# Optimization experiments

Hardware: AMD Instinct MI355X
Metric: run time of the kernel (lower is better)

## Reference

```python
import jax, jax.numpy as jnp
import numpy as np

IN_F = 4096
OUT_F = 4096
B, S = 4, 2048
RMS_EPS = 1e-6
Q_EPS = 1e-5


def setup_inputs() -> dict:
    key = jax.random.key(0)
    kx, kw, kb, ks = jax.random.split(key, 4)
    x = jax.random.normal(kx, (B, S, IN_F), dtype=jnp.float32)
    # ternary BitNet weight in {-1, 0, +1}, stored as float32 for the reference
    W = (jax.random.randint(kw, (OUT_F, IN_F), 0, 3) - 1).astype(jnp.float32)
    rms_weight = jnp.ones((IN_F,), dtype=jnp.float32)
    bias = jax.random.normal(kb, (OUT_F,), dtype=jnp.float32)
    weight_scale = jax.random.uniform(ks, (1,), dtype=jnp.float32) + 0.5
    return {"x": x, "W": W, "rms_weight": rms_weight, "bias": bias,
            "weight_scale": weight_scale}


def reference(x, W, rms_weight, bias, weight_scale):
    # RMSNorm (self.rms_norm applied before quantized matmul)
    var = jnp.mean(x * x, axis=-1, keepdims=True)
    h = x * jax.lax.rsqrt(var + RMS_EPS) * rms_weight
    # BitNet act_quant: per-token absmax int8 quantization
    scale = 127.0 / jnp.clip(jnp.max(jnp.abs(h), axis=-1, keepdims=True), Q_EPS)  # [B,S,1]
    q = jnp.clip(jnp.round(h * scale), -128.0, 127.0)
    # ternary GEMV per token, then dequant
    y = jnp.einsum('bsk,ok->bso', q, W) / scale  # [B,S,OUT_F]
    y = y + bias
    y = y * weight_scale  # weight_scale_mode == 'multiply'
    return y
```

## Files before the change

### kernel.cpp

```cpp
#include <hip/hip_runtime.h>

#define IN_F 4096
#define OUT_F 4096
#define NTOK 8192
#define KDIM 4096

using i32x4 = __attribute__((ext_vector_type(4))) int;
using f32x4 = __attribute__((ext_vector_type(4))) float;

__device__ __forceinline__ void gload_lds16(const void* g, void* l) {
  __builtin_amdgcn_global_load_lds(
      (const __attribute__((address_space(1))) void*)g,
      (__attribute__((address_space(3))) void*)l, 16, 0, 0);
}

#define WAITV(n) asm volatile("s_waitcnt vmcnt(" #n ")" ::: "memory")
#define BAR() do { asm volatile("" ::: "memory"); __builtin_amdgcn_s_barrier(); \
                   asm volatile("" ::: "memory"); } while (0)

__global__ __launch_bounds__(256) void rmsq_kernel(
    const float* __restrict__ x, const float* __restrict__ rmsw,
    signed char* __restrict__ q, float* __restrict__ dscale) {
  const int tok = blockIdx.x;
  const int tid = threadIdx.x;
  const f32x4* xr = (const f32x4*)(x + (size_t)tok * IN_F);
  const f32x4* wr = (const f32x4*)rmsw;

  f32x4 v[4];
  float ss = 0.f;
#pragma unroll
  for (int c = 0; c < 4; ++c) {
    v[c] = xr[c * 256 + tid];
    ss += v[c].x * v[c].x + v[c].y * v[c].y + v[c].z * v[c].z + v[c].w * v[c].w;
  }

  __shared__ float red[4];
#pragma unroll
  for (int off = 32; off > 0; off >>= 1) ss += __shfl_down(ss, off, 64);
  const int wid = tid >> 6;
  if ((tid & 63) == 0) red[wid] = ss;
  __syncthreads();
  const float tot = red[0] + red[1] + red[2] + red[3];
  const float rinv = rsqrtf(tot * (1.0f / IN_F) + 1e-6f);

  f32x4 h[4];
  float amax = 0.f;
#pragma unroll
  for (int c = 0; c < 4; ++c) {
    f32x4 w = wr[c * 256 + tid];
    h[c].x = v[c].x * rinv * w.x;
    h[c].y = v[c].y * rinv * w.y;
    h[c].z = v[c].z * rinv * w.z;
    h[c].w = v[c].w * rinv * w.w;
    amax = fmaxf(amax, fabsf(h[c].x));
    amax = fmaxf(amax, fabsf(h[c].y));
    amax = fmaxf(amax, fabsf(h[c].z));
    amax = fmaxf(amax, fabsf(h[c].w));
  }

  __syncthreads();
#pragma unroll
  for (int off = 32; off > 0; off >>= 1)
    amax = fmaxf(amax, __shfl_down(amax, off, 64));
  if ((tid & 63) == 0) red[wid] = amax;
  __syncthreads();
  amax = fmaxf(fmaxf(red[0], red[1]), fmaxf(red[2], red[3]));
  amax = fmaxf(amax, 1e-5f);
  const float qs = 127.0f / amax;
  if (tid == 0) dscale[tok] = amax * (1.0f / 127.0f);

  uint* qo = (uint*)(q + (size_t)tok * IN_F);
#pragma unroll
  for (int c = 0; c < 4; ++c) {
    float r0 = fminf(fmaxf(rintf(h[c].x * qs), -128.f), 127.f);
    float r1 = fminf(fmaxf(rintf(h[c].y * qs), -128.f), 127.f);
    float r2 = fminf(fmaxf(rintf(h[c].z * qs), -128.f), 127.f);
    float r3 = fminf(fmaxf(rintf(h[c].w * qs), -128.f), 127.f);
    uint p = ((uint)((int)r0 & 255)) | ((uint)((int)r1 & 255) << 8) |
             ((uint)((int)r2 & 255) << 16) | ((uint)((int)r3 & 255) << 24);
    qo[c * 256 + tid] = p;
  }
}

__global__ __launch_bounds__(256) void wconv_kernel(
    const float* __restrict__ W, signed char* __restrict__ Wq) {
  const int idx = blockIdx.x * 256 + threadIdx.x;
  f32x4 w = ((const f32x4*)W)[idx];
  uint p = ((uint)((int)w.x & 255)) | ((uint)((int)w.y & 255) << 8) |
           ((uint)((int)w.z & 255) << 16) | ((uint)((int)w.w & 255) << 24);
  ((uint*)Wq)[idx] = p;
}

#define BM 128
#define BN 256
#define BK 64
#define NT (KDIM / BK)
#define ATILEB (BM * BK)
#define BTILEB (BN * BK)
#define BUFB (ATILEB + BTILEB)
#define NBUF 3

__global__ __launch_bounds__(256, 2) void gemm_kernel(
    const signed char* __restrict__ A, const signed char* __restrict__ Bw,
    const float* __restrict__ dscale, const float* __restrict__ bias,
    const float* __restrict__ wscale_p, float* __restrict__ out) {
  __shared__ __align__(16) signed char lds[NBUF * BUFB];

  const int tid = threadIdx.x;
  const int lane = tid & 63;
  const int wc = tid >> 6;

  const int bid = blockIdx.x;
  const int swz = (bid & 7) * 128 + (bid >> 3);
  const int m0 = (swz & 63) * BM;
  const int n0 = (swz >> 6) * BN;

  const int cA0 = tid, cA1 = tid + 256;
  const int rA0 = cA0 >> 2, rA1 = cA1 >> 2;
  const int sA0 = (cA0 & 3) ^ ((rA0 >> 1) & 3);
  const int sA1 = (cA1 & 3) ^ ((rA1 >> 1) & 3);
  const signed char* agp0 = A + (size_t)(m0 + rA0) * KDIM + sA0 * 16;
  const signed char* agp1 = A + (size_t)(m0 + rA1) * KDIM + sA1 * 16;
  const int rB = tid >> 2;
  const signed char* bgp[4];
#pragma unroll
  for (int j = 0; j < 4; ++j) {
    const int rBj = rB + j * 64;
    const int sBj = (tid & 3) ^ ((rBj >> 1) & 3);
    bgp[j] = Bw + (size_t)(n0 + rBj) * KDIM + sBj * 16;
  }

#define STAGE(kt, boff)                                                    \
  do {                                                                     \
    const int k0_ = (kt) * BK;                                             \
    signed char* lb_ = &lds[(boff)];                                       \
    gload_lds16(agp0 + k0_, lb_ + cA0 * 16);                               \
    gload_lds16(agp1 + k0_, lb_ + cA1 * 16);                               \
    gload_lds16(bgp[0] + k0_, lb_ + ATILEB + (tid + 0 * 256) * 16);        \
    gload_lds16(bgp[1] + k0_, lb_ + ATILEB + (tid + 1 * 256) * 16);        \
    gload_lds16(bgp[2] + k0_, lb_ + ATILEB + (tid + 2 * 256) * 16);        \
    gload_lds16(bgp[3] + k0_, lb_ + ATILEB + (tid + 3 * 256) * 16);        \
  } while (0)

  const int fr = lane & 15;
  const int ks = lane >> 4;
  int offA[8], offB[4];
#pragma unroll
  for (int mi = 0; mi < 8; ++mi) {
    const int row = mi * 16 + fr;
    offA[mi] = row * BK + ((ks ^ ((row >> 1) & 3)) * 16);
  }
#pragma unroll
  for (int ni = 0; ni < 4; ++ni) {
    const int row = wc * 64 + ni * 16 + fr;
    offB[ni] = ATILEB + row * BK + ((ks ^ ((row >> 1) & 3)) * 16);
  }

  i32x4 acc[8][4];
#pragma unroll
  for (int i = 0; i < 8; ++i)
#pragma unroll
    for (int j = 0; j < 4; ++j) acc[i][j] = (i32x4){0, 0, 0, 0};

  STAGE(0, 0);
  STAGE(1, BUFB);

  int br = 0;
  int bs = 2 * BUFB;
  for (int t = 0; t < NT; ++t) {
    if (t < NT - 1) WAITV(6); else WAITV(0);
    BAR();

    const signed char* bp = &lds[br];
    i32x4 af[8], bf[4];
#pragma unroll
    for (int mi = 0; mi < 8; ++mi) af[mi] = *(const i32x4*)(bp + offA[mi]);
#pragma unroll
    for (int ni = 0; ni < 4; ++ni) bf[ni] = *(const i32x4*)(bp + offB[ni]);

    if (t + 2 < NT) STAGE(t + 2, bs);

    __builtin_amdgcn_s_setprio(1);
#pragma unroll
    for (int mi = 0; mi < 8; ++mi)
#pragma unroll
      for (int ni = 0; ni < 4; ++ni)
        acc[mi][ni] = __builtin_amdgcn_mfma_i32_16x16x64_i8(af[mi], bf[ni],
                                                            acc[mi][ni], 0, 0, 0);
    __builtin_amdgcn_s_setprio(0);

    br += BUFB; if (br == NBUF * BUFB) br = 0;
    bs += BUFB; if (bs == NBUF * BUFB) bs = 0;
  }

  const float wsc = wscale_p[0];
  const int rbase = (lane >> 4) * 4;
  float bv[4];
#pragma unroll
  for (int ni = 0; ni < 4; ++ni) bv[ni] = bias[n0 + wc * 64 + ni * 16 + fr];
#pragma unroll
  for (int mi = 0; mi < 8; ++mi) {
#pragma unroll
    for (int r = 0; r < 4; ++r) {
      const int m = m0 + mi * 16 + rbase + r;
      const float ds = dscale[m];
      float* orow = out + (size_t)m * OUT_F + n0 + wc * 64;
#pragma unroll
      for (int ni = 0; ni < 4; ++ni) {
        orow[ni * 16 + fr] = ((float)acc[mi][ni][r] * ds + bv[ni]) * wsc;
      }
    }
  }
#undef STAGE
}

extern "C" void kernel_launch(void* const* d_in, const int* in_sizes, int n_in,
                              void* d_out, int out_size, void* d_ws, size_t ws_size,
                              hipStream_t stream) {
  const float* x = (const float*)d_in[0];
  const float* W = (const float*)d_in[1];
  const float* rmsw = (const float*)d_in[2];
  const float* bias = (const float*)d_in[3];
  const float* wscale = (const float*)d_in[4];
  float* out = (float*)d_out;

  signed char* q = (signed char*)d_ws;
  signed char* Wq = q + (size_t)NTOK * IN_F;
  float* dscale = (float*)(Wq + (size_t)OUT_F * IN_F);

  rmsq_kernel<<<NTOK, 256, 0, stream>>>(x, rmsw, q, dscale);
  wconv_kernel<<<(OUT_F * IN_F / 4) / 256, 256, 0, stream>>>(W, Wq);
  gemm_kernel<<<(NTOK / BM) * (OUT_F / BN), 256, 0, stream>>>(q, Wq, dscale,
                                                              bias, wscale, out);
}
```

Baseline: 192.0 us.

## Load B fragments directly from global into registers, stage only A in LDS

Each wave reads a disjoint 64-row slice of the weight tile, so staging B through shared memory gave no reuse. The change drops B from LDS and loads each wave's B fragments straight from global memory into registers, prefetched one k-step ahead. The freed LDS gives the A tile a fourth buffer and a three-stage prefetch. This removes the LDS write and read traffic for B. In exchange, global-load latency is exposed with only one iteration of lookahead, and the B loads are small, scattered 16-byte-per-lane reads that rely on cache hits.

```diff
diff --git a/kernel.cpp b/kernel.cpp
--- a/kernel.cpp
+++ b/kernel.cpp
@@ -96,15 +96,13 @@
 #define BK 64
 #define NT (KDIM / BK)
 #define ATILEB (BM * BK)
-#define BTILEB (BN * BK)
-#define BUFB (ATILEB + BTILEB)
-#define NBUF 3
+#define NBUF 4
 
 __global__ __launch_bounds__(256, 2) void gemm_kernel(
     const signed char* __restrict__ A, const signed char* __restrict__ Bw,
     const float* __restrict__ dscale, const float* __restrict__ bias,
     const float* __restrict__ wscale_p, float* __restrict__ out) {
-  __shared__ __align__(16) signed char lds[NBUF * BUFB];
+  __shared__ __align__(16) signed char lds[NBUF * ATILEB];
 
   const int tid = threadIdx.x;
   const int lane = tid & 63;
@@ -121,40 +119,28 @@
   const int sA1 = (cA1 & 3) ^ ((rA1 >> 1) & 3);
   const signed char* agp0 = A + (size_t)(m0 + rA0) * KDIM + sA0 * 16;
   const signed char* agp1 = A + (size_t)(m0 + rA1) * KDIM + sA1 * 16;
-  const int rB = tid >> 2;
-  const signed char* bgp[4];
-#pragma unroll
-  for (int j = 0; j < 4; ++j) {
-    const int rBj = rB + j * 64;
-    const int sBj = (tid & 3) ^ ((rBj >> 1) & 3);
-    bgp[j] = Bw + (size_t)(n0 + rBj) * KDIM + sBj * 16;
-  }
-
-#define STAGE(kt, boff)                                                    \
+
+#define STAGE_A(kt, boff)                                                  \
   do {                                                                     \
     const int k0_ = (kt) * BK;                                             \
     signed char* lb_ = &lds[(boff)];                                       \
     gload_lds16(agp0 + k0_, lb_ + cA0 * 16);                               \
     gload_lds16(agp1 + k0_, lb_ + cA1 * 16);                               \
-    gload_lds16(bgp[0] + k0_, lb_ + ATILEB + (tid + 0 * 256) * 16);        \
-    gload_lds16(bgp[1] + k0_, lb_ + ATILEB + (tid + 1 * 256) * 16);        \
-    gload_lds16(bgp[2] + k0_, lb_ + ATILEB + (tid + 2 * 256) * 16);        \
-    gload_lds16(bgp[3] + k0_, lb_ + ATILEB + (tid + 3 * 256) * 16);        \
   } while (0)
 
   const int fr = lane & 15;
   const int ks = lane >> 4;
-  int offA[8], offB[4];
+  int offA[8];
 #pragma unroll
   for (int mi = 0; mi < 8; ++mi) {
     const int row = mi * 16 + fr;
     offA[mi] = row * BK + ((ks ^ ((row >> 1) & 3)) * 16);
   }
-#pragma unroll
-  for (int ni = 0; ni < 4; ++ni) {
-    const int row = wc * 64 + ni * 16 + fr;
-    offB[ni] = ATILEB + row * BK + ((ks ^ ((row >> 1) & 3)) * 16);
-  }
+
+  const signed char* bgl[4];
+#pragma unroll
+  for (int ni = 0; ni < 4; ++ni)
+    bgl[ni] = Bw + (size_t)(n0 + wc * 64 + ni * 16 + fr) * KDIM + ks * 16;
 
   i32x4 acc[8][4];
 #pragma unroll
@@ -162,35 +148,49 @@
 #pragma unroll
     for (int j = 0; j < 4; ++j) acc[i][j] = (i32x4){0, 0, 0, 0};
 
-  STAGE(0, 0);
-  STAGE(1, BUFB);
+  STAGE_A(0, 0);
+  STAGE_A(1, ATILEB);
+  STAGE_A(2, 2 * ATILEB);
+  i32x4 bcur0 = *(const i32x4*)(bgl[0]);
+  i32x4 bcur1 = *(const i32x4*)(bgl[1]);
+  i32x4 bcur2 = *(const i32x4*)(bgl[2]);
+  i32x4 bcur3 = *(const i32x4*)(bgl[3]);
 
   int br = 0;
-  int bs = 2 * BUFB;
+  int bs = 3 * ATILEB;
   for (int t = 0; t < NT; ++t) {
-    if (t < NT - 1) WAITV(6); else WAITV(0);
+    WAITV(8);
     BAR();
 
     const signed char* bp = &lds[br];
-    i32x4 af[8], bf[4];
+    i32x4 af[8];
 #pragma unroll
     for (int mi = 0; mi < 8; ++mi) af[mi] = *(const i32x4*)(bp + offA[mi]);
-#pragma unroll
-    for (int ni = 0; ni < 4; ++ni) bf[ni] = *(const i32x4*)(bp + offB[ni]);
-
-    if (t + 2 < NT) STAGE(t + 2, bs);
+
+    i32x4 bn0, bn1, bn2, bn3;
+    if (t + 1 < NT) {
+      const int ko = (t + 1) * BK;
+      bn0 = *(const i32x4*)(bgl[0] + ko);
+      bn1 = *(const i32x4*)(bgl[1] + ko);
+      bn2 = *(const i32x4*)(bgl[2] + ko);
+      bn3 = *(const i32x4*)(bgl[3] + ko);
+    }
+
+    if (t + 3 < NT) STAGE_A(t + 3, bs);
 
     __builtin_amdgcn_s_setprio(1);
 #pragma unroll
-    for (int mi = 0; mi < 8; ++mi)
-#pragma unroll
-      for (int ni = 0; ni < 4; ++ni)
-        acc[mi][ni] = __builtin_amdgcn_mfma_i32_16x16x64_i8(af[mi], bf[ni],
-                                                            acc[mi][ni], 0, 0, 0);
+    for (int mi = 0; mi < 8; ++mi) {
+      acc[mi][0] = __builtin_amdgcn_mfma_i32_16x16x64_i8(af[mi], bcur0, acc[mi][0], 0, 0, 0);
+      acc[mi][1] = __builtin_amdgcn_mfma_i32_16x16x64_i8(af[mi], bcur1, acc[mi][1], 0, 0, 0);
+      acc[mi][2] = __builtin_amdgcn_mfma_i32_16x16x64_i8(af[mi], bcur2, acc[mi][2], 0, 0, 0);
+      acc[mi][3] = __builtin_amdgcn_mfma_i32_16x16x64_i8(af[mi], bcur3, acc[mi][3], 0, 0, 0);
+    }
     __builtin_amdgcn_s_setprio(0);
 
-    br += BUFB; if (br == NBUF * BUFB) br = 0;
-    bs += BUFB; if (bs == NBUF * BUFB) bs = 0;
+    bcur0 = bn0; bcur1 = bn1; bcur2 = bn2; bcur3 = bn3;
+    br += ATILEB; if (br == NBUF * ATILEB) br = 0;
+    bs += ATILEB; if (bs == NBUF * ATILEB) bs = 0;
   }
 
   const float wsc = wscale_p[0];
@@ -211,7 +211,7 @@
       }
     }
   }
-#undef STAGE
+#undef STAGE_A
 }
 
 extern "C" void kernel_launch(void* const* d_in, const int* in_sizes, int n_in,
```

New measurement: 224.5 us. 16.9% more time.

## Use two waves per GEMM block with 128x128 warp tiles

Applied to the files above, without the earlier changes.

The GEMM block drops from four waves to two, so each wave now computes a 128x128 output tile (8x8 MFMA accumulators) instead of 128x64. Each thread issues twice as many global-to-LDS loads per stage, and the vmcnt wait is adjusted to match. The aim is more MFMA work per LDS fragment read and fewer LDS reads overall. In exchange, accumulator register use doubles (256 VGPRs of accumulators alone), which may force use of AGPRs or spilling, and fewer waves are resident to hide latency.

```diff
diff --git a/kernel.cpp b/kernel.cpp
--- a/kernel.cpp
+++ b/kernel.cpp
@@ -100,7 +100,7 @@
 #define BUFB (ATILEB + BTILEB)
 #define NBUF 3
 
-__global__ __launch_bounds__(256, 2) void gemm_kernel(
+__global__ __launch_bounds__(128, 1) void gemm_kernel(
     const signed char* __restrict__ A, const signed char* __restrict__ Bw,
     const float* __restrict__ dscale, const float* __restrict__ bias,
     const float* __restrict__ wscale_p, float* __restrict__ out) {
@@ -115,52 +115,60 @@
   const int m0 = (swz & 63) * BM;
   const int n0 = (swz >> 6) * BN;
 
-  const int cA0 = tid, cA1 = tid + 256;
-  const int rA0 = cA0 >> 2, rA1 = cA1 >> 2;
-  const int sA0 = (cA0 & 3) ^ ((rA0 >> 1) & 3);
-  const int sA1 = (cA1 & 3) ^ ((rA1 >> 1) & 3);
-  const signed char* agp0 = A + (size_t)(m0 + rA0) * KDIM + sA0 * 16;
-  const signed char* agp1 = A + (size_t)(m0 + rA1) * KDIM + sA1 * 16;
-  const int rB = tid >> 2;
-  const signed char* bgp[4];
+  const signed char* agp[4];
 #pragma unroll
   for (int j = 0; j < 4; ++j) {
-    const int rBj = rB + j * 64;
-    const int sBj = (tid & 3) ^ ((rBj >> 1) & 3);
-    bgp[j] = Bw + (size_t)(n0 + rBj) * KDIM + sBj * 16;
+    const int u = tid + j * 128;
+    const int r = u >> 2;
+    const int s = (u & 3) ^ ((r >> 1) & 3);
+    agp[j] = A + (size_t)(m0 + r) * KDIM + s * 16;
+  }
+  const signed char* bgp[8];
+#pragma unroll
+  for (int j = 0; j < 8; ++j) {
+    const int u = tid + j * 128;
+    const int r = u >> 2;
+    const int s = (u & 3) ^ ((r >> 1) & 3);
+    bgp[j] = Bw + (size_t)(n0 + r) * KDIM + s * 16;
   }
 
 #define STAGE(kt, boff)                                                    \
   do {                                                                     \
     const int k0_ = (kt) * BK;                                             \
     signed char* lb_ = &lds[(boff)];                                       \
-    gload_lds16(agp0 + k0_, lb_ + cA0 * 16);                               \
-    gload_lds16(agp1 + k0_, lb_ + cA1 * 16);                               \
-    gload_lds16(bgp[0] + k0_, lb_ + ATILEB + (tid + 0 * 256) * 16);        \
-    gload_lds16(bgp[1] + k0_, lb_ + ATILEB + (tid + 1 * 256) * 16);        \
-    gload_lds16(bgp[2] + k0_, lb_ + ATILEB + (tid + 2 * 256) * 16);        \
-    gload_lds16(bgp[3] + k0_, lb_ + ATILEB + (tid + 3 * 256) * 16);        \
+    gload_lds16(agp[0] + k0_, lb_ + (tid + 0 * 128) * 16);                 \
+    gload_lds16(agp[1] + k0_, lb_ + (tid + 1 * 128) * 16);                 \
+    gload_lds16(agp[2] + k0_, lb_ + (tid + 2 * 128) * 16);                 \
+    gload_lds16(agp[3] + k0_, lb_ + (tid + 3 * 128) * 16);                 \
+    gload_lds16(bgp[0] + k0_, lb_ + ATILEB + (tid + 0 * 128) * 16);        \
+    gload_lds16(bgp[1] + k0_, lb_ + ATILEB + (tid + 1 * 128) * 16);        \
+    gload_lds16(bgp[2] + k0_, lb_ + ATILEB + (tid + 2 * 128) * 16);        \
+    gload_lds16(bgp[3] + k0_, lb_ + ATILEB + (tid + 3 * 128) * 16);        \
+    gload_lds16(bgp[4] + k0_, lb_ + ATILEB + (tid + 4 * 128) * 16);        \
+    gload_lds16(bgp[5] + k0_, lb_ + ATILEB + (tid + 5 * 128) * 16);        \
+    gload_lds16(bgp[6] + k0_, lb_ + ATILEB + (tid + 6 * 128) * 16);        \
+    gload_lds16(bgp[7] + k0_, lb_ + ATILEB + (tid + 7 * 128) * 16);        \
   } while (0)
 
   const int fr = lane & 15;
   const int ks = lane >> 4;
-  int offA[8], offB[4];
+  int offA[8], offB[8];
 #pragma unroll
   for (int mi = 0; mi < 8; ++mi) {
     const int row = mi * 16 + fr;
-    offA[mi] = row * BK + ((ks ^ ((row >> 1) & 3)) * 16);
-  }
-#pragma unroll
-  for (int ni = 0; ni < 4; ++ni) {
-    const int row = wc * 64 + ni * 16 + fr;
-    offB[ni] = ATILEB + row * BK + ((ks ^ ((row >> 1) & 3)) * 16);
-  }
-
-  i32x4 acc[8][4];
+    offA[mi] = (row * 4 + (ks ^ ((row >> 1) & 3))) * 16;
+  }
+#pragma unroll
+  for (int ni = 0; ni < 8; ++ni) {
+    const int row = wc * 128 + ni * 16 + fr;
+    offB[ni] = ATILEB + (row * 4 + (ks ^ ((row >> 1) & 3))) * 16;
+  }
+
+  i32x4 acc[8][8];
 #pragma unroll
   for (int i = 0; i < 8; ++i)
 #pragma unroll
-    for (int j = 0; j < 4; ++j) acc[i][j] = (i32x4){0, 0, 0, 0};
+    for (int j = 0; j < 8; ++j) acc[i][j] = (i32x4){0, 0, 0, 0};
 
   STAGE(0, 0);
   STAGE(1, BUFB);
@@ -168,15 +176,15 @@
   int br = 0;
   int bs = 2 * BUFB;
   for (int t = 0; t < NT; ++t) {
-    if (t < NT - 1) WAITV(6); else WAITV(0);
+    if (t < NT - 1) WAITV(12); else WAITV(0);
     BAR();
 
     const signed char* bp = &lds[br];
-    i32x4 af[8], bf[4];
-#pragma unroll
-    for (int mi = 0; mi < 8; ++mi) af[mi] = *(const i32x4*)(bp + offA[mi]);
-#pragma unroll
-    for (int ni = 0; ni < 4; ++ni) bf[ni] = *(const i32x4*)(bp + offB[ni]);
+    i32x4 af[8], bf[8];
+#pragma unroll
+    for (int i = 0; i < 8; ++i) af[i] = *(const i32x4*)(bp + offA[i]);
+#pragma unroll
+    for (int i = 0; i < 8; ++i) bf[i] = *(const i32x4*)(bp + offB[i]);
 
     if (t + 2 < NT) STAGE(t + 2, bs);
 
@@ -184,7 +192,7 @@
 #pragma unroll
     for (int mi = 0; mi < 8; ++mi)
 #pragma unroll
-      for (int ni = 0; ni < 4; ++ni)
+      for (int ni = 0; ni < 8; ++ni)
         acc[mi][ni] = __builtin_amdgcn_mfma_i32_16x16x64_i8(af[mi], bf[ni],
                                                             acc[mi][ni], 0, 0, 0);
     __builtin_amdgcn_s_setprio(0);
@@ -195,18 +203,18 @@
 
   const float wsc = wscale_p[0];
   const int rbase = (lane >> 4) * 4;
-  float bv[4];
-#pragma unroll
-  for (int ni = 0; ni < 4; ++ni) bv[ni] = bias[n0 + wc * 64 + ni * 16 + fr];
+  float bv[8];
+#pragma unroll
+  for (int ni = 0; ni < 8; ++ni) bv[ni] = bias[n0 + wc * 128 + ni * 16 + fr];
 #pragma unroll
   for (int mi = 0; mi < 8; ++mi) {
 #pragma unroll
     for (int r = 0; r < 4; ++r) {
       const int m = m0 + mi * 16 + rbase + r;
       const float ds = dscale[m];
-      float* orow = out + (size_t)m * OUT_F + n0 + wc * 64;
-#pragma unroll
-      for (int ni = 0; ni < 4; ++ni) {
+      float* orow = out + (size_t)m * OUT_F + n0 + wc * 128;
+#pragma unroll
+      for (int ni = 0; ni < 8; ++ni) {
         orow[ni * 16 + fr] = ((float)acc[mi][ni][r] * ds + bv[ni]) * wsc;
       }
     }
@@ -230,6 +238,6 @@
 
   rmsq_kernel<<<NTOK, 256, 0, stream>>>(x, rmsw, q, dscale);
   wconv_kernel<<<(OUT_F * IN_F / 4) / 256, 256, 0, stream>>>(W, Wq);
-  gemm_kernel<<<(NTOK / BM) * (OUT_F / BN), 256, 0, stream>>>(q, Wq, dscale,
+  gemm_kernel<<<(NTOK / BM) * (OUT_F / BN), 128, 0, stream>>>(q, Wq, dscale,
                                                               bias, wscale, out);
 }
```

Measured after the change: 193.1 us. No clear change (+0.6%).
